# Kernel optimization log

Measured on AMD Instinct MI355X. Metric: run time of the kernel, lower is better.

## Reference

```python
import jax, jax.numpy as jnp
import numpy as np

N, C, H, W = 16, 128, 48, 48
CI = C // 2  # inter_channels


def setup_inputs() -> dict:
    key = jax.random.key(0)
    ks = jax.random.split(key, 9)
    s_in = 1.0 / np.sqrt(C)
    s_out = 1.0 / np.sqrt(CI)
    return {
        "features": jax.random.normal(ks[0], (N, C, H, W), jnp.float32),
        "Wq": jax.random.normal(ks[1], (CI, C), jnp.float32) * s_in,
        "bq": jax.random.normal(ks[2], (CI,), jnp.float32) * 0.01,
        "Wk": jax.random.normal(ks[3], (CI, C), jnp.float32) * s_in,
        "bk": jax.random.normal(ks[4], (CI,), jnp.float32) * 0.01,
        "Wv": jax.random.normal(ks[5], (CI, C), jnp.float32) * s_in,
        "bv": jax.random.normal(ks[6], (CI,), jnp.float32) * 0.01,
        "Wz": jax.random.normal(ks[7], (C, CI), jnp.float32) * s_out,
        "bz": jax.random.normal(ks[8], (C,), jnp.float32) * 0.01,
    }


def reference(features, Wq, bq, Wk, bk, Wv, bv, Wz, bz):
    n, c, h, w = features.shape
    hw = h * w

    def proj(x, Wp, bp):
        # conv1x1 over (n, c, h, w) -> tokens (n, hw, ci)
        t = jnp.einsum('nchw,dc->ndhw', x, Wp) + bp[None, :, None, None]
        return t.reshape(n, -1, hw).transpose(0, 2, 1)

    q = proj(features, Wq, bq)   # (n, hw, ci)
    k = proj(features, Wk, bk)
    v = proj(features, Wv, bv)

    # before/after neighbor slices with edge clamping (slice 0 / slice n-1 use themselves)
    kb = jnp.concatenate([k[:1], k[:-1]], axis=0)
    vb = jnp.concatenate([v[:1], v[:-1]], axis=0)
    ka = jnp.concatenate([k[1:], k[-1:]], axis=0)
    va = jnp.concatenate([v[1:], v[-1:]], axis=0)

    def attend(kk, vv):
        f = jnp.einsum('nqd,nkd->nqk', q, kk)        # (n, hw, hw); no 1/sqrt(d) scale, per original
        a = jax.nn.softmax(f, axis=-1)
        y = jnp.einsum('nqk,nkd->nqd', a, vv)        # (n, hw, ci)
        z = jnp.einsum('nqd,cd->nqc', y, Wz) + bz    # W_z conv1x1
        return z.transpose(0, 2, 1).reshape(n, c, h, w)

    return attend(kb, vb) + attend(ka, va) + features
```

## Files before the change

### kernel.cpp

```cpp
#include <hip/hip_runtime.h>
#include <math.h>

#define NBATCH 16
#define CCH    128
#define HW     2304
#define DI     64
#define NTILE  36
#define HTILE  18
#define QBLK   18

typedef unsigned short u16;
typedef unsigned int   u32;
typedef __bf16   bf16x8 __attribute__((ext_vector_type(8)));
typedef _Float16 f16x8  __attribute__((ext_vector_type(8)));
typedef float    f32x4  __attribute__((ext_vector_type(4)));

__device__ __forceinline__ u16 f2bf_rne(float x) {
    union { float f; u32 u; } v; v.f = x;
    u32 r = (v.u + 0x7FFFu + ((v.u >> 16) & 1u)) >> 16;
    return (u16)r;
}
__device__ __forceinline__ u16 f2h(float x) {
    union { _Float16 h; u16 u; } c; c.h = (_Float16)x; return c.u;
}
__device__ __forceinline__ u32 pkh(float a, float b) {
    union { _Float16 h[2]; u32 u; } c; c.h[0] = (_Float16)a; c.h[1] = (_Float16)b; return c.u;
}
__device__ __forceinline__ float h0f(u32 w) { union { u32 u; _Float16 h[2]; } c; c.u = w; return (float)c.h[0]; }
__device__ __forceinline__ float h1f(u32 w) { union { u32 u; _Float16 h[2]; } c; c.u = w; return (float)c.h[1]; }

__global__ __launch_bounds__(256) void wprep_kernel(
    const float* __restrict__ Wq, const float* __restrict__ Wk,
    const float* __restrict__ Wv, const float* __restrict__ Wz,
    u16* __restrict__ Wf, u16* __restrict__ Wzf)
{
    const int idx  = blockIdx.x * 256 + threadIdx.x;
    if (idx < 3072) {
        const int lane = idx & 63;
        const int fi   = idx >> 6;
        const int g = fi >> 2, ks = fi & 3;
        const int lo = lane & 15, hi = lane >> 4;
        const int row = g * 16 + lo;
        const float* src = (row < 64)  ? &Wq[row * CCH]
                         : (row < 128) ? &Wk[(row - 64) * CCH]
                                       : &Wv[(row - 128) * CCH];
        const int c0 = (ks * 4 + hi) * 8;
        float4 a = *(const float4*)&src[c0];
        float4 b = *(const float4*)&src[c0 + 4];
        union { u16 s8[8]; uint4 v; } pk;
        pk.s8[0] = f2h(a.x); pk.s8[1] = f2h(a.y); pk.s8[2] = f2h(a.z); pk.s8[3] = f2h(a.w);
        pk.s8[4] = f2h(b.x); pk.s8[5] = f2h(b.y); pk.s8[6] = f2h(b.z); pk.s8[7] = f2h(b.w);
        *(uint4*)&Wf[(size_t)idx * 8] = pk.v;
    } else {
        const int t    = idx - 3072;
        const int lane = t & 63;
        const int fi   = t >> 6;
        const int g = fi >> 1, ks = fi & 1;
        const int lo = lane & 15, hi = lane >> 4;
        const int row = g * 16 + lo;
        const int d0  = ks * 32 + hi * 8;
        float4 a = *(const float4*)&Wz[row * DI + d0];
        float4 b = *(const float4*)&Wz[row * DI + d0 + 4];
        union { u16 s8[8]; uint4 v; } pk;
        pk.s8[0] = f2h(a.x); pk.s8[1] = f2h(a.y); pk.s8[2] = f2h(a.z); pk.s8[3] = f2h(a.w);
        pk.s8[4] = f2h(b.x); pk.s8[5] = f2h(b.y); pk.s8[6] = f2h(b.z); pk.s8[7] = f2h(b.w);
        *(uint4*)&Wzf[(size_t)t * 8] = pk.v;
    }
}

__global__ __launch_bounds__(256) void proj_kernel(
    const float* __restrict__ F, const u16* __restrict__ Wf,
    const float* __restrict__ bq, const float* __restrict__ bk,
    const float* __restrict__ bv,
    u16* __restrict__ qo, u16* __restrict__ ko, u16* __restrict__ vto)
{
    __shared__ __align__(16) u16 Fl[64 * 128];
    __shared__ __align__(16) u16 Vt[64 * 72];

    const int tid  = threadIdx.x;
    const int n    = blockIdx.x / NTILE;
    const int p0   = (blockIdx.x % NTILE) * 64;
    const int lane = tid & 63, wave = tid >> 6;
    const int lo   = lane & 15, hi = lane >> 4;

    const float* Fn = F + (size_t)n * CCH * HW;
    #pragma unroll
    for (int i = 0; i < 4; ++i) {
        int s  = tid + i * 256;
        int c0 = (s >> 4) * 2;
        int t0 = (s & 15) * 4;
        const float* fp_ = &Fn[(size_t)c0 * HW + p0 + t0];
        float4 fa = *(const float4*)fp_;
        float4 fb = *(const float4*)(fp_ + HW);
        #pragma unroll
        for (int e = 0; e < 4; ++e) {
            int t = t0 + e;
            u32 w = (u32)f2h((&fa.x)[e]) | ((u32)f2h((&fb.x)[e]) << 16);
            *(u32*)&Fl[t * 128 + (((c0 >> 3) ^ (t & 15)) << 3) + (c0 & 7)] = w;
        }
    }
    __syncthreads();

    const int arow = wave * 16 + lo;
    f16x8 af[4];
    #pragma unroll
    for (int ks = 0; ks < 4; ++ks)
        af[ks] = *(const f16x8*)&Fl[arow * 128 + (((ks * 4 + hi) ^ lo) << 3)];

    f32x4 acc[12];
    #pragma unroll
    for (int g = 0; g < 12; ++g)
        #pragma unroll
        for (int r = 0; r < 4; ++r) acc[g][r] = 0.f;

    #pragma unroll
    for (int g = 0; g < 12; ++g) {
        #pragma unroll
        for (int ks = 0; ks < 4; ++ks) {
            f16x8 bf = *(const f16x8*)&Wf[(size_t)((g * 4 + ks) * 64 + lane) * 8];
            acc[g] = __builtin_amdgcn_mfma_f32_16x16x32_f16(af[ks], bf, acc[g], 0, 0, 0);
        }
    }

    const int twb = p0 + wave * 16 + 4 * hi;
    #pragma unroll
    for (int g = 0; g < 4; ++g) {
        float bQ = bq[g * 16 + lo], bK = bk[g * 16 + lo];
        #pragma unroll
        for (int r = 0; r < 4; ++r) {
            size_t off = ((size_t)n * HW + twb + r) * DI + g * 16 + lo;
            qo[off] = f2h(acc[g][r] + bQ);
            ko[off] = f2h(acc[g + 4][r] + bK);
        }
    }
    #pragma unroll
    for (int g = 0; g < 4; ++g) {
        float bV = bv[g * 16 + lo];
        #pragma unroll
        for (int r = 0; r < 4; ++r)
            Vt[(g * 16 + lo) * 72 + wave * 16 + 4 * hi + r] = f2bf_rne(acc[g + 8][r] + bV);
    }
    __syncthreads();
    #pragma unroll
    for (int i = 0; i < 2; ++i) {
        int s = tid + i * 256;
        int d = s >> 3, c8 = (s & 7) * 8;
        *(uint4*)&vto[((size_t)n * DI + d) * HW + p0 + c8] = *(const uint4*)&Vt[d * 72 + c8];
    }
}

__global__ __launch_bounds__(512, 2) void attn_pass_kernel(
    const u16* __restrict__ q, const u16* __restrict__ k, const u16* __restrict__ vt,
    u16* __restrict__ ypart)
{
    __shared__ __align__(16) u16 smem[32768];
    const int tid  = threadIdx.x;
    const int lane = tid & 63;
    const int wave = tid >> 6;
    const int w4   = wave & 3;
    const int half = wave >> 2;
    const int lo   = lane & 15, hi = lane >> 4;

    const int bid  = (int)blockIdx.x;
    const int w    = (bid & 7) * 72 + (bid >> 3);
    const int pass = w / (NBATCH * QBLK);
    const int rem  = w % (NBATCH * QBLK);
    const int n    = rem / QBLK;
    const int p0   = (rem % QBLK) * 128;

    const int nb = (pass == 0) ? (n > 0 ? n - 1 : 0)
                               : (n < NBATCH - 1 ? n + 1 : n);
    const u16* kp = k  + (size_t)nb * HW * DI;
    const u16* vp = vt + (size_t)nb * DI * HW;
    const int  kq = half * (HTILE * 64);

    u16* const Kb0 = smem + half * 8192;
    u16* const Kb1 = Kb0 + 4096;
    u16* const Vb0 = smem + 16384 + half * 8192;
    u16* const Vb1 = Vb0 + 4096;

    f16x8 qfA0, qfA1, qfB0, qfB1;
    {
        const u16* qp = q + ((size_t)n * HW + p0 + w4 * 32 + lo) * DI + hi * 8;
        qfA0 = *(const f16x8*)qp;
        qfA1 = *(const f16x8*)(qp + 32);
        qfB0 = *(const f16x8*)(qp + 16 * DI);
        qfB1 = *(const f16x8*)(qp + 16 * DI + 32);
    }

    const int stid  = tid & 255;
    const int sch   = stid & 7;
    const int srow0 = stid >> 3;
    const int srow1 = srow0 + 32;
    const int fk0   = (srow0 & 3) | ((srow0 & 8) >> 1);
    const int fk1   = (srow1 & 3) | ((srow1 & 8) >> 1);
    const int koff0 = srow0 * 64 + ((sch ^ fk0) * 8);
    const int koff1 = srow1 * 64 + ((sch ^ fk1) * 8);
    const int voff0 = srow0 * 64 + ((sch ^ (srow0 & 7)) * 8);
    const int voff1 = srow1 * 64 + ((sch ^ (srow1 & 7)) * 8);

    const int krbase = 8 * (lo >> 2) + (lo & 3);
    const int xl = lo & 7;

    f32x4 yaccA[4], yaccB[4];
    #pragma unroll
    for (int nf = 0; nf < 4; ++nf)
        #pragma unroll
        for (int r = 0; r < 4; ++r) { yaccA[nf][r] = 0.f; yaccB[nf][r] = 0.f; }
    float laccA = 0.f, laccB = 0.f;

    uint4 ka0 = *(const uint4*)(kp + (size_t)(kq + srow0) * DI + sch * 8);
    uint4 ka1 = *(const uint4*)(kp + (size_t)(kq + srow1) * DI + sch * 8);
    uint4 va0 = *(const uint4*)(vp + (size_t)srow0 * HW + kq + sch * 8);
    uint4 va1 = *(const uint4*)(vp + (size_t)srow1 * HW + kq + sch * 8);
    *(uint4*)&Kb0[koff0] = ka0;  *(uint4*)&Kb0[koff1] = ka1;
    *(uint4*)&Vb0[voff0] = va0;  *(uint4*)&Vb0[voff1] = va1;
    ka0 = *(const uint4*)(kp + (size_t)(kq + 64 + srow0) * DI + sch * 8);
    ka1 = *(const uint4*)(kp + (size_t)(kq + 64 + srow1) * DI + sch * 8);
    va0 = *(const uint4*)(vp + (size_t)srow0 * HW + kq + 64 + sch * 8);
    va1 = *(const uint4*)(vp + (size_t)srow1 * HW + kq + 64 + sch * 8);
    __syncthreads();

    auto body = [&](int t, const u16* Kc, const u16* Vc, u16* Kn, u16* Vn) {
        f32x4 stA[4], stB[4];
        __builtin_amdgcn_s_setprio(1);
        #pragma unroll
        for (int m = 0; m < 4; ++m) {
            const int kr = krbase + 4 * (m & 1) + 32 * (m >> 1);
            f16x8 a0 = *(const f16x8*)&Kc[kr * 64 + ((hi ^ xl) * 8)];
            f16x8 a1 = *(const f16x8*)&Kc[kr * 64 + (((4 + hi) ^ xl) * 8)];
            f32x4 zA = {0.f, 0.f, 0.f, 0.f};
            zA = __builtin_amdgcn_mfma_f32_16x16x32_f16(a0, qfA0, zA, 0, 0, 0);
            zA = __builtin_amdgcn_mfma_f32_16x16x32_f16(a1, qfA1, zA, 0, 0, 0);
            stA[m] = zA;
            f32x4 zB = {0.f, 0.f, 0.f, 0.f};
            zB = __builtin_amdgcn_mfma_f32_16x16x32_f16(a0, qfB0, zB, 0, 0, 0);
            zB = __builtin_amdgcn_mfma_f32_16x16x32_f16(a1, qfB1, zB, 0, 0, 0);
            stB[m] = zB;
        }
        __builtin_amdgcn_s_setprio(0);

        bf16x8 paA0, paA1, paB0, paB1;
        #pragma unroll
        for (int m = 0; m < 4; ++m) {
            float e0 = __expf(stA[m][0]);
            float e1 = __expf(stA[m][1]);
            float e2 = __expf(stA[m][2]);
            float e3 = __expf(stA[m][3]);
            laccA += (e0 + e1) + (e2 + e3);
            __bf16 b0 = (__bf16)e0, b1 = (__bf16)e1, b2 = (__bf16)e2, b3 = (__bf16)e3;
            if (m == 0)      { paA0[0] = b0; paA0[1] = b1; paA0[2] = b2; paA0[3] = b3; }
            else if (m == 1) { paA0[4] = b0; paA0[5] = b1; paA0[6] = b2; paA0[7] = b3; }
            else if (m == 2) { paA1[0] = b0; paA1[1] = b1; paA1[2] = b2; paA1[3] = b3; }
            else             { paA1[4] = b0; paA1[5] = b1; paA1[6] = b2; paA1[7] = b3; }
        }
        #pragma unroll
        for (int m = 0; m < 4; ++m) {
            float e0 = __expf(stB[m][0]);
            float e1 = __expf(stB[m][1]);
            float e2 = __expf(stB[m][2]);
            float e3 = __expf(stB[m][3]);
            laccB += (e0 + e1) + (e2 + e3);
            __bf16 b0 = (__bf16)e0, b1 = (__bf16)e1, b2 = (__bf16)e2, b3 = (__bf16)e3;
            if (m == 0)      { paB0[0] = b0; paB0[1] = b1; paB0[2] = b2; paB0[3] = b3; }
            else if (m == 1) { paB0[4] = b0; paB0[5] = b1; paB0[6] = b2; paB0[7] = b3; }
            else if (m == 2) { paB1[0] = b0; paB1[1] = b1; paB1[2] = b2; paB1[3] = b3; }
            else             { paB1[4] = b0; paB1[5] = b1; paB1[6] = b2; paB1[7] = b3; }
        }

        __builtin_amdgcn_s_setprio(1);
        #pragma unroll
        for (int nf = 0; nf < 4; ++nf) {
            const int vr = nf * 16 + lo;
            bf16x8 v0 = *(const bf16x8*)&Vc[vr * 64 + ((hi ^ xl) * 8)];
            bf16x8 v1 = *(const bf16x8*)&Vc[vr * 64 + (((4 + hi) ^ xl) * 8)];
            yaccA[nf] = __builtin_amdgcn_mfma_f32_16x16x32_bf16(paA0, v0, yaccA[nf], 0, 0, 0);
            yaccA[nf] = __builtin_amdgcn_mfma_f32_16x16x32_bf16(paA1, v1, yaccA[nf], 0, 0, 0);
            yaccB[nf] = __builtin_amdgcn_mfma_f32_16x16x32_bf16(paB0, v0, yaccB[nf], 0, 0, 0);
            yaccB[nf] = __builtin_amdgcn_mfma_f32_16x16x32_bf16(paB1, v1, yaccB[nf], 0, 0, 0);
        }
        __builtin_amdgcn_s_setprio(0);

        if (t + 1 < HTILE) {
            *(uint4*)&Kn[koff0] = ka0; *(uint4*)&Kn[koff1] = ka1;
            *(uint4*)&Vn[voff0] = va0; *(uint4*)&Vn[voff1] = va1;
        }
        if (t + 2 < HTILE) {
            int tb = kq + (t + 2) * 64;
            ka0 = *(const uint4*)(kp + (size_t)(tb + srow0) * DI + sch * 8);
            ka1 = *(const uint4*)(kp + (size_t)(tb + srow1) * DI + sch * 8);
            va0 = *(const uint4*)(vp + (size_t)srow0 * HW + tb + sch * 8);
            va1 = *(const uint4*)(vp + (size_t)srow1 * HW + tb + sch * 8);
        }
        __syncthreads();
    };

    #pragma unroll 1
    for (int tt = 0; tt < HTILE; tt += 2) {
        body(tt,     Kb0, Vb0, Kb1, Vb1);
        body(tt + 1, Kb1, Vb1, Kb0, Vb0);
    }

    float lA = laccA;
    lA += __shfl_xor(lA, 16);
    lA += __shfl_xor(lA, 32);
    float lB = laccB;
    lB += __shfl_xor(lB, 16);
    lB += __shfl_xor(lB, 32);

    float* Ll = (float*)smem;
    u32*   X  = (u32*)((char*)smem + 4096);
    u16*   yw = smem + 10240;

    if (hi == 0) {
        Ll[((half * 4 + w4) * 2 + 0) * 16 + lo] = lA;
        Ll[((half * 4 + w4) * 2 + 1) * 16 + lo] = lB;
    }
    __syncthreads();

    float sA[4], sB[4];
    #pragma unroll
    for (int r = 0; r < 4; ++r) {
        int qr = 4 * hi + r;
        sA[r] = 1.f / (Ll[((0 * 4 + w4) * 2 + 0) * 16 + qr] + Ll[((1 * 4 + w4) * 2 + 0) * 16 + qr]);
        sB[r] = 1.f / (Ll[((0 * 4 + w4) * 2 + 1) * 16 + qr] + Ll[((1 * 4 + w4) * 2 + 1) * 16 + qr]);
    }
    float zA[4][4], zB[4][4];
    #pragma unroll
    for (int nf = 0; nf < 4; ++nf)
        #pragma unroll
        for (int r = 0; r < 4; ++r) {
            zA[nf][r] = yaccA[nf][r] * sA[r];
            zB[nf][r] = yaccB[nf][r] * sB[r];
        }

    u32* Xl = &X[(w4 * 64 + lane) * 16];
    if (half == 1) {
        #pragma unroll
        for (int nf = 0; nf < 4; ++nf) {
            Xl[nf * 2 + 0]     = pkh(zA[nf][0], zA[nf][1]);
            Xl[nf * 2 + 1]     = pkh(zA[nf][2], zA[nf][3]);
            Xl[8 + nf * 2 + 0] = pkh(zB[nf][0], zB[nf][1]);
            Xl[8 + nf * 2 + 1] = pkh(zB[nf][2], zB[nf][3]);
        }
    }
    __syncthreads();

    if (half == 0) {
        #pragma unroll
        for (int nf = 0; nf < 4; ++nf) {
            u32 wa0 = Xl[nf * 2 + 0], wa1 = Xl[nf * 2 + 1];
            u32 wb0 = Xl[8 + nf * 2 + 0], wb1 = Xl[8 + nf * 2 + 1];
            zA[nf][0] += h0f(wa0); zA[nf][1] += h1f(wa0);
            zA[nf][2] += h0f(wa1); zA[nf][3] += h1f(wa1);
            zB[nf][0] += h0f(wb0); zB[nf][1] += h1f(wb0);
            zB[nf][2] += h0f(wb1); zB[nf][3] += h1f(wb1);
        }
        #pragma unroll
        for (int nf = 0; nf < 4; ++nf)
            #pragma unroll
            for (int r = 0; r < 4; ++r) {
                yw[(w4 * 32 + 4 * hi + r) * 72 + nf * 16 + lo]      = f2h(zA[nf][r]);
                yw[(w4 * 32 + 16 + 4 * hi + r) * 72 + nf * 16 + lo] = f2h(zB[nf][r]);
            }
    }
    __syncthreads();

    u16* yg = ypart + ((size_t)(pass * NBATCH + n) * HW + p0) * DI;
    #pragma unroll
    for (int s = 0; s < 2; ++s) {
        int idx = tid + s * 512;
        int row = idx >> 3, c8 = (idx & 7) * 8;
        *(uint4*)&yg[row * DI + c8] = *(const uint4*)&yw[row * 72 + c8];
    }
}

__global__ __launch_bounds__(256) void combine_kernel(
    const u16* __restrict__ ypart, const u16* __restrict__ Wzf,
    const float* __restrict__ bz, const float* __restrict__ F,
    float* __restrict__ out)
{
    __shared__ __align__(16) float zs[64 * 129];
    const int tid  = threadIdx.x;
    const int n    = blockIdx.x / NTILE;
    const int p0   = (blockIdx.x % NTILE) * 64;
    const int lane = tid & 63, wave = tid >> 6;
    const int lo   = lane & 15, hi = lane >> 4;

    const u16* y0 = ypart + ((size_t)n * HW + p0 + wave * 16 + lo) * DI;
    const u16* y1 = ypart + ((size_t)(NBATCH + n) * HW + p0 + wave * 16 + lo) * DI;
    f16x8 a00 = *(const f16x8*)(y0 + hi * 8);
    f16x8 a01 = *(const f16x8*)(y0 + 32 + hi * 8);
    f16x8 a10 = *(const f16x8*)(y1 + hi * 8);
    f16x8 a11 = *(const f16x8*)(y1 + 32 + hi * 8);

    f32x4 acc[8];
    #pragma unroll
    for (int g = 0; g < 8; ++g)
        #pragma unroll
        for (int r = 0; r < 4; ++r) acc[g][r] = 0.f;

    #pragma unroll
    for (int g = 0; g < 8; ++g) {
        f16x8 b0 = *(const f16x8*)&Wzf[(size_t)((g * 2 + 0) * 64 + lane) * 8];
        f16x8 b1 = *(const f16x8*)&Wzf[(size_t)((g * 2 + 1) * 64 + lane) * 8];
        acc[g] = __builtin_amdgcn_mfma_f32_16x16x32_f16(a00, b0, acc[g], 0, 0, 0);
        acc[g] = __builtin_amdgcn_mfma_f32_16x16x32_f16(a01, b1, acc[g], 0, 0, 0);
        acc[g] = __builtin_amdgcn_mfma_f32_16x16x32_f16(a10, b0, acc[g], 0, 0, 0);
        acc[g] = __builtin_amdgcn_mfma_f32_16x16x32_f16(a11, b1, acc[g], 0, 0, 0);
    }

    #pragma unroll
    for (int g = 0; g < 8; ++g)
        #pragma unroll
        for (int r = 0; r < 4; ++r)
            zs[(wave * 16 + 4 * hi + r) * 129 + g * 16 + lo] = acc[g][r];
    __syncthreads();

    #pragma unroll 4
    for (int i = 0; i < 32; ++i) {
        int c = wave + 4 * i;
        size_t gi = (size_t)(n * CCH + c) * HW + p0 + lane;
        out[gi] = zs[lane * 129 + c] + 2.f * bz[c] + F[gi];
    }
}

extern "C" void kernel_launch(void* const* d_in, const int* in_sizes, int n_in,
                              void* d_out, int out_size, void* d_ws, size_t ws_size,
                              hipStream_t stream) {
    const float* F  = (const float*)d_in[0];
    const float* Wq = (const float*)d_in[1];
    const float* bq = (const float*)d_in[2];
    const float* Wk = (const float*)d_in[3];
    const float* bk = (const float*)d_in[4];
    const float* Wv = (const float*)d_in[5];
    const float* bv = (const float*)d_in[6];
    const float* Wz = (const float*)d_in[7];
    const float* bz = (const float*)d_in[8];
    float* outp = (float*)d_out;

    const size_t tok = (size_t)NBATCH * HW * DI;
    u16* qb  = (u16*)d_ws;
    u16* kb  = qb  + tok;
    u16* vtb = kb  + tok;
    u16* yp  = vtb + tok;
    u16* wf  = yp  + 2 * tok;
    u16* wzf = wf  + 24576;

    wprep_kernel<<<16, 256, 0, stream>>>(Wq, Wk, Wv, Wz, wf, wzf);
    proj_kernel<<<NBATCH * NTILE, 256, 0, stream>>>(F, wf, bq, bk, bv, qb, kb, vtb);
    attn_pass_kernel<<<2 * NBATCH * QBLK, 512, 0, stream>>>(qb, kb, vtb, yp);
    combine_kernel<<<NBATCH * NTILE, 256, 0, stream>>>(yp, wzf, bz, F, outp);
}
```

Before: 96.98 us.

## Split attention KV halves into separate blocks and merge partials in combine kernel

The attention kernel no longer runs the two KV halves as wave groups inside one 512-thread block. Each half is now its own 256-thread block, which doubles the grid and halves shared memory per block. Each block writes its normalized partial output (fp16) and its softmax row-sum to global memory, using the output buffer as scratch, and the combine kernel reweights and merges the partials before the Wz projection. This removes the in-block cross-half reduction and its syncs and should raise occupancy. In exchange, more intermediate data goes through global memory, and the merge precision changes because the weights are fp16.

```diff
diff --git a/kernel.cpp b/kernel.cpp
--- a/kernel.cpp
+++ b/kernel.cpp
@@ -23,11 +23,6 @@
 __device__ __forceinline__ u16 f2h(float x) {
     union { _Float16 h; u16 u; } c; c.h = (_Float16)x; return c.u;
 }
-__device__ __forceinline__ u32 pkh(float a, float b) {
-    union { _Float16 h[2]; u32 u; } c; c.h[0] = (_Float16)a; c.h[1] = (_Float16)b; return c.u;
-}
-__device__ __forceinline__ float h0f(u32 w) { union { u32 u; _Float16 h[2]; } c; c.u = w; return (float)c.h[0]; }
-__device__ __forceinline__ float h1f(u32 w) { union { u32 u; _Float16 h[2]; } c; c.u = w; return (float)c.h[1]; }
 
 __global__ __launch_bounds__(256) void wprep_kernel(
     const float* __restrict__ Wq, const float* __restrict__ Wk,
@@ -149,24 +144,29 @@
     }
 }
 
-__global__ __launch_bounds__(512, 2) void attn_pass_kernel(
+__global__ __launch_bounds__(256) void attn_pass_kernel(
     const u16* __restrict__ q, const u16* __restrict__ k, const u16* __restrict__ vt,
-    u16* __restrict__ ypart)
+    float* __restrict__ outF, float* __restrict__ lp)
 {
-    __shared__ __align__(16) u16 smem[32768];
+    __shared__ __align__(16) u16 smem[16384];
+    u16* const Kb0 = smem;
+    u16* const Kb1 = smem + 4096;
+    u16* const Vb0 = smem + 8192;
+    u16* const Vb1 = smem + 12288;
+
     const int tid  = threadIdx.x;
     const int lane = tid & 63;
-    const int wave = tid >> 6;
-    const int w4   = wave & 3;
-    const int half = wave >> 2;
+    const int w4   = tid >> 6;
     const int lo   = lane & 15, hi = lane >> 4;
 
     const int bid  = (int)blockIdx.x;
-    const int w    = (bid & 7) * 72 + (bid >> 3);
-    const int pass = w / (NBATCH * QBLK);
+    const int w    = (bid & 7) * 144 + (bid >> 3);
+    const int j    = w / (NBATCH * QBLK);
     const int rem  = w % (NBATCH * QBLK);
     const int n    = rem / QBLK;
-    const int p0   = (rem % QBLK) * 128;
+    const int qb   = rem % QBLK;
+    const int pass = j >> 1, half = j & 1;
+    const int P0   = qb * 128;
 
     const int nb = (pass == 0) ? (n > 0 ? n - 1 : 0)
                                : (n < NBATCH - 1 ? n + 1 : n);
@@ -174,23 +174,17 @@
     const u16* vp = vt + (size_t)nb * DI * HW;
     const int  kq = half * (HTILE * 64);
 
-    u16* const Kb0 = smem + half * 8192;
-    u16* const Kb1 = Kb0 + 4096;
-    u16* const Vb0 = smem + 16384 + half * 8192;
-    u16* const Vb1 = Vb0 + 4096;
-
     f16x8 qfA0, qfA1, qfB0, qfB1;
     {
-        const u16* qp = q + ((size_t)n * HW + p0 + w4 * 32 + lo) * DI + hi * 8;
+        const u16* qp = q + ((size_t)n * HW + P0 + w4 * 32 + lo) * DI + hi * 8;
         qfA0 = *(const f16x8*)qp;
         qfA1 = *(const f16x8*)(qp + 32);
         qfB0 = *(const f16x8*)(qp + 16 * DI);
         qfB1 = *(const f16x8*)(qp + 16 * DI + 32);
     }
 
-    const int stid  = tid & 255;
-    const int sch   = stid & 7;
-    const int srow0 = stid >> 3;
+    const int sch   = tid & 7;
+    const int srow0 = tid >> 3;
     const int srow1 = srow0 + 32;
     const int fk0   = (srow0 & 3) | ((srow0 & 8) >> 1);
     const int fk1   = (srow1 & 3) | ((srow1 & 8) >> 1);
@@ -307,78 +301,46 @@
     float lB = laccB;
     lB += __shfl_xor(lB, 16);
     lB += __shfl_xor(lB, 32);
-
-    float* Ll = (float*)smem;
-    u32*   X  = (u32*)((char*)smem + 4096);
-    u16*   yw = smem + 10240;
+    float invA = 1.f / lA, invB = 1.f / lB;
+    float invqA[4], invqB[4];
+    #pragma unroll
+    for (int r = 0; r < 4; ++r) {
+        invqA[r] = __shfl(invA, 20 * hi + r);
+        invqB[r] = __shfl(invB, 20 * hi + r);
+    }
 
     if (hi == 0) {
-        Ll[((half * 4 + w4) * 2 + 0) * 16 + lo] = lA;
-        Ll[((half * 4 + w4) * 2 + 1) * 16 + lo] = lB;
-    }
-    __syncthreads();
-
-    float sA[4], sB[4];
-    #pragma unroll
-    for (int r = 0; r < 4; ++r) {
-        int qr = 4 * hi + r;
-        sA[r] = 1.f / (Ll[((0 * 4 + w4) * 2 + 0) * 16 + qr] + Ll[((1 * 4 + w4) * 2 + 0) * 16 + qr]);
-        sB[r] = 1.f / (Ll[((0 * 4 + w4) * 2 + 1) * 16 + qr] + Ll[((1 * 4 + w4) * 2 + 1) * 16 + qr]);
-    }
-    float zA[4][4], zB[4][4];
+        lp[((size_t)j * NBATCH + n) * HW + P0 + w4 * 32 + lo]      = lA;
+        lp[((size_t)j * NBATCH + n) * HW + P0 + w4 * 32 + 16 + lo] = lB;
+    }
+
+    __syncthreads();
+    u16* yw = smem;
     #pragma unroll
     for (int nf = 0; nf < 4; ++nf)
         #pragma unroll
         for (int r = 0; r < 4; ++r) {
-            zA[nf][r] = yaccA[nf][r] * sA[r];
-            zB[nf][r] = yaccB[nf][r] * sB[r];
-        }
-
-    u32* Xl = &X[(w4 * 64 + lane) * 16];
-    if (half == 1) {
-        #pragma unroll
-        for (int nf = 0; nf < 4; ++nf) {
-            Xl[nf * 2 + 0]     = pkh(zA[nf][0], zA[nf][1]);
-            Xl[nf * 2 + 1]     = pkh(zA[nf][2], zA[nf][3]);
-            Xl[8 + nf * 2 + 0] = pkh(zB[nf][0], zB[nf][1]);
-            Xl[8 + nf * 2 + 1] = pkh(zB[nf][2], zB[nf][3]);
-        }
-    }
-    __syncthreads();
-
-    if (half == 0) {
-        #pragma unroll
-        for (int nf = 0; nf < 4; ++nf) {
-            u32 wa0 = Xl[nf * 2 + 0], wa1 = Xl[nf * 2 + 1];
-            u32 wb0 = Xl[8 + nf * 2 + 0], wb1 = Xl[8 + nf * 2 + 1];
-            zA[nf][0] += h0f(wa0); zA[nf][1] += h1f(wa0);
-            zA[nf][2] += h0f(wa1); zA[nf][3] += h1f(wa1);
-            zB[nf][0] += h0f(wb0); zB[nf][1] += h1f(wb0);
-            zB[nf][2] += h0f(wb1); zB[nf][3] += h1f(wb1);
-        }
-        #pragma unroll
-        for (int nf = 0; nf < 4; ++nf)
-            #pragma unroll
-            for (int r = 0; r < 4; ++r) {
-                yw[(w4 * 32 + 4 * hi + r) * 72 + nf * 16 + lo]      = f2h(zA[nf][r]);
-                yw[(w4 * 32 + 16 + 4 * hi + r) * 72 + nf * 16 + lo] = f2h(zB[nf][r]);
-            }
-    }
-    __syncthreads();
-
-    u16* yg = ypart + ((size_t)(pass * NBATCH + n) * HW + p0) * DI;
-    #pragma unroll
-    for (int s = 0; s < 2; ++s) {
-        int idx = tid + s * 512;
-        int row = idx >> 3, c8 = (idx & 7) * 8;
-        *(uint4*)&yg[row * DI + c8] = *(const uint4*)&yw[row * 72 + c8];
+            yw[(w4 * 32 + 4 * hi + r) * 72 + nf * 16 + lo]      = f2h(yaccA[nf][r] * invqA[r]);
+            yw[(w4 * 32 + 16 + 4 * hi + r) * 72 + nf * 16 + lo] = f2h(yaccB[nf][r] * invqB[r]);
+        }
+    __syncthreads();
+
+    u32* outb = (u32*)outF + (size_t)n * CCH * HW + (size_t)j * 32 * HW;
+    const int ptb = P0 >> 6;
+    #pragma unroll
+    for (int s = 0; s < 4; ++s) {
+        int idx = tid + s * 256;
+        int T   = idx >> 3, d0 = (idx & 7) * 8;
+        int tok = T & 63;
+        int f   = (tok >> 1) * HW + (ptb + (T >> 6)) * 64 + (tok & 1) * 32 + (d0 >> 1);
+        *(uint4*)&outb[f] = *(const uint4*)&yw[T * 72 + d0];
     }
 }
 
 __global__ __launch_bounds__(256) void combine_kernel(
-    const u16* __restrict__ ypart, const u16* __restrict__ Wzf,
-    const float* __restrict__ bz, const float* __restrict__ F,
-    float* __restrict__ out)
+    float* __restrict__ outF, const float* __restrict__ lp,
+    const u16* __restrict__ Wzf, const float* __restrict__ bz,
+    const float* __restrict__ F)
 {
     __shared__ __align__(16) float zs[64 * 129];
     const int tid  = threadIdx.x;
@@ -386,13 +348,28 @@
     const int p0   = (blockIdx.x % NTILE) * 64;
     const int lane = tid & 63, wave = tid >> 6;
     const int lo   = lane & 15, hi = lane >> 4;
-
-    const u16* y0 = ypart + ((size_t)n * HW + p0 + wave * 16 + lo) * DI;
-    const u16* y1 = ypart + ((size_t)(NBATCH + n) * HW + p0 + wave * 16 + lo) * DI;
-    f16x8 a00 = *(const f16x8*)(y0 + hi * 8);
-    f16x8 a01 = *(const f16x8*)(y0 + 32 + hi * 8);
-    f16x8 a10 = *(const f16x8*)(y1 + hi * 8);
-    f16x8 a11 = *(const f16x8*)(y1 + 32 + hi * 8);
+    const int tok  = wave * 16 + lo;
+
+    const u32* pb = (const u32*)outF + (size_t)n * CCH * HW;
+    f16x8 af[4][2];
+    #pragma unroll
+    for (int jj = 0; jj < 4; ++jj)
+        #pragma unroll
+        for (int ks = 0; ks < 2; ++ks)
+            af[jj][ks] = *(const f16x8*)&pb[(size_t)(jj * 32 + (tok >> 1)) * HW
+                                            + p0 + (tok & 1) * 32 + ks * 16 + hi * 4];
+    float lw[4];
+    #pragma unroll
+    for (int jj = 0; jj < 4; ++jj)
+        lw[jj] = lp[((size_t)jj * NBATCH + n) * HW + p0 + tok];
+    float s0 = 1.f / (lw[0] + lw[1]);
+    float s1 = 1.f / (lw[2] + lw[3]);
+    _Float16 w00 = (_Float16)(lw[0] * s0), w01 = (_Float16)(lw[1] * s0);
+    _Float16 w10 = (_Float16)(lw[2] * s1), w11 = (_Float16)(lw[3] * s1);
+    f16x8 a00 = af[0][0] * w00 + af[1][0] * w01;
+    f16x8 a01 = af[0][1] * w00 + af[1][1] * w01;
+    f16x8 a10 = af[2][0] * w10 + af[3][0] * w11;
+    f16x8 a11 = af[2][1] * w10 + af[3][1] * w11;
 
     f32x4 acc[8];
     #pragma unroll
@@ -421,7 +398,7 @@
     for (int i = 0; i < 32; ++i) {
         int c = wave + 4 * i;
         size_t gi = (size_t)(n * CCH + c) * HW + p0 + lane;
-        out[gi] = zs[lane * 129 + c] + 2.f * bz[c] + F[gi];
+        outF[gi] = zs[lane * 129 + c] + 2.f * bz[c] + F[gi];
     }
 }
 
@@ -440,15 +417,15 @@
     float* outp = (float*)d_out;
 
     const size_t tok = (size_t)NBATCH * HW * DI;
-    u16* qb  = (u16*)d_ws;
-    u16* kb  = qb  + tok;
-    u16* vtb = kb  + tok;
-    u16* yp  = vtb + tok;
-    u16* wf  = yp  + 2 * tok;
-    u16* wzf = wf  + 24576;
+    u16*   qb  = (u16*)d_ws;
+    u16*   kb  = qb  + tok;
+    u16*   vtb = kb  + tok;
+    u16*   wf  = vtb + tok;
+    u16*   wzf = wf  + 24576;
+    float* lpb = (float*)(wzf + 8192);
 
     wprep_kernel<<<16, 256, 0, stream>>>(Wq, Wk, Wv, Wz, wf, wzf);
     proj_kernel<<<NBATCH * NTILE, 256, 0, stream>>>(F, wf, bq, bk, bv, qb, kb, vtb);
-    attn_pass_kernel<<<2 * NBATCH * QBLK, 512, 0, stream>>>(qb, kb, vtb, yp);
-    combine_kernel<<<NBATCH * NTILE, 256, 0, stream>>>(yp, wzf, bz, F, outp);
-}
+    attn_pass_kernel<<<4 * NBATCH * QBLK, 256, 0, stream>>>(qb, kb, vtb, outp, lpb);
+    combine_kernel<<<NBATCH * NTILE, 256, 0, stream>>>(outp, lpb, wzf, bz, F);
+}
```

Result: faster. 94.84 us (-2.2%).
